# Kernel tuning notes

Hardware: AMD Instinct MI355X
Metric: run time of the kernel (lower is better)

The kernel has to match this reference:

```python
import jax, jax.numpy as jnp
import numpy as np


def setup_inputs() -> dict:
    key = jax.random.key(0)
    k1, k2, k3 = jax.random.split(key, 3)
    B, T, C, H, W = 8, 30, 4, 256, 256
    images = jax.random.normal(k1, (B, T, C, H, W), dtype=jnp.float32)
    # 1 = occluded, 0 = visible (per docstring)
    cloud_mask = jax.random.bernoulli(k2, 0.5, (B, T, 1, H, W)).astype(jnp.float32)
    # strictly increasing acquisition days per batch element
    days = jnp.cumsum(jax.random.randint(k3, (B, T), 1, 10), axis=1).astype(jnp.float32)
    return {"images": images, "cloud_mask": cloud_mask, "days": days}


def _interpolate(images, cloud_mask, days):
    # images: (B,T,C,H,W), cloud_mask: (B,T,1,H,W), days: (B,T)
    B, T, C, H, W = images.shape
    visible = cloud_mask[:, :, 0, :, :] == 0.0                  # (B,T,H,W)
    t_idx = jnp.arange(T, dtype=jnp.int32)[None, :, None, None]

    # last-visible index: running max over time of (t if visible else -1); -1 == never seen yet (NaN in ref)
    lv = jax.lax.cummax(jnp.where(visible, t_idx, -1), axis=1)
    # next-visible index: reverse running min of (t if visible else T); T == never seen again (NaN in ref)
    nv = jax.lax.cummin(jnp.where(visible, t_idx, T), axis=1, reverse=True)

    lv_ok = lv >= 0
    nv_ok = nv < T
    lv_c = jnp.clip(lv, 0, T - 1)
    nv_c = jnp.clip(nv, 0, T - 1)

    def gather_img(idx):  # idx: (B,T,H,W) int -> (B,T,C,H,W)
        full = jnp.broadcast_to(idx[:, :, None, :, :], (B, T, C, H, W))
        return jnp.take_along_axis(images, full, axis=1)

    def gather_day(idx):  # idx: (B,T,H,W) int -> (B,T,H,W)
        return jnp.take_along_axis(days, idx.reshape(B, -1), axis=1).reshape(B, T, H, W)

    img_last = gather_img(lv_c)
    img_next = gather_img(nv_c)
    d_last = gather_day(lv_c)
    d_next = gather_day(nv_c)
    d_t = jnp.broadcast_to(days[:, :, None, None], (B, T, H, W))

    denom = d_next - d_last
    frac = (d_t - d_last) / jnp.where(denom == 0.0, 1.0, denom)  # safe; denom==0 only where visible
    interp = img_last + frac[:, :, None, :, :] * (img_next - img_last)

    vis_c = visible[:, :, None, :, :]
    both = (lv_ok & nv_ok)[:, :, None, :, :]
    only_last = (lv_ok & ~nv_ok)[:, :, None, :, :]
    only_next = (~lv_ok & nv_ok)[:, :, None, :, :]
    nan = jnp.float32(jnp.nan)

    out = jnp.where(vis_c, images,
          jnp.where(both, interp,
          jnp.where(only_last, img_last,
          jnp.where(only_next, img_next, nan))))
    return out


def reference(images, cloud_mask, days):
    return _interpolate(images, cloud_mask, days)
```

## Files before the change

### kernel.cpp

```cpp
#include <hip/hip_runtime.h>

namespace {

constexpr int T   = 30;
constexpr int C   = 4;
constexpr int HW  = 256 * 256;
constexpr int B   = 8;
constexpr int CHW = C * HW;

typedef _Float16 f16x2 __attribute__((ext_vector_type(2)));

__global__ __attribute__((amdgpu_flat_work_group_size(256, 256)))
           __attribute__((amdgpu_waves_per_eu(4, 4)))
void interp_kernel(
    const float* __restrict__ images,
    const float* __restrict__ mask,
    const float* __restrict__ days,
    float* __restrict__ out)
{
    __shared__ float s_day[T];
    const int tid = threadIdx.x;
    const int b   = blockIdx.x >> 8;
    if (tid < T) s_day[tid] = days[b * T + tid];
    __syncthreads();

    const int hw = ((blockIdx.x & 255) << 8) | tid;

    const float* mbase = mask + (size_t)b * T * HW + hw;
    unsigned vis = 0u;
    {
        float mv[T];
#pragma unroll
        for (int t = 0; t < T; ++t) mv[t] = mbase[(size_t)t * HW];
        __builtin_amdgcn_sched_barrier(0);
#pragma unroll
        for (int t = 0; t < T; ++t) vis |= (mv[t] == 0.0f ? 1u : 0u) << t;
    }

    f16x2 fr[T / 2];
    {
        float run = 0.0f;
#pragma unroll
        for (int t = T - 1; t >= 0; --t) {
            run = ((vis >> t) & 1u) ? s_day[t] : run;
            if (t & 1) fr[t >> 1].y = (_Float16)run;
            else       fr[t >> 1].x = (_Float16)run;
        }
        float dl = 0.0f;
#pragma unroll
        for (int t = 0; t < T; ++t) {
            const float d = s_day[t];
            dl = ((vis >> t) & 1u) ? d : dl;
            const float dn = (t & 1) ? (float)fr[t >> 1].y
                                     : (float)fr[t >> 1].x;
            float den = dn - dl;
            den = (den == 0.0f) ? 1.0f : den;
            float f = (d - dl) / den;
            const bool lv_ok = (vis & ((1u << (t + 1)) - 1u)) != 0u;
            const bool nv_ok = (vis >> t) != 0u;
            f = (lv_ok && nv_ok) ? f : (nv_ok ? 1.0f : 0.0f);
            if (t & 1) fr[t >> 1].y = (_Float16)f;
            else       fr[t >> 1].x = (_Float16)f;
        }
    }

    const bool  none = (vis == 0u);
    const float nanv = __int_as_float(0x7fc00000);
    const size_t pixBase = (size_t)b * T * CHW + hw;

#pragma unroll 1
    for (int c = 0; c < C; ++c) {
        const float* ib = images + pixBase + (size_t)c * HW;
        float*       ob = out    + pixBase + (size_t)c * HW;

        float v[T];
#pragma unroll
        for (int t = 0; t < T; ++t) v[t] = ib[(size_t)t * CHW];
        __builtin_amdgcn_sched_barrier(0);

        f16x2 nvp[T / 2];
        {
            float run = 0.0f;
#pragma unroll
            for (int t = T - 1; t >= 0; --t) {
                run = ((vis >> t) & 1u) ? v[t] : run;
                if (t & 1) nvp[t >> 1].y = (_Float16)run;
                else       nvp[t >> 1].x = (_Float16)run;
            }
        }
        {
            float rl = 0.0f;
#pragma unroll
            for (int t = 0; t < T; ++t) {
                const float nv = (t & 1) ? (float)nvp[t >> 1].y
                                         : (float)nvp[t >> 1].x;
                rl = ((vis >> t) & 1u) ? nv : rl;
                const float f  = (t & 1) ? (float)fr[t >> 1].y
                                         : (float)fr[t >> 1].x;
                const float res = fmaf(f, nv - rl, rl);
                __builtin_nontemporal_store(none ? nanv : res,
                                            &ob[(size_t)t * CHW]);
            }
        }
    }
}

}

extern "C" void kernel_launch(void* const* d_in, const int* in_sizes, int n_in,
                              void* d_out, int out_size, void* d_ws, size_t ws_size,
                              hipStream_t stream)
{
    const float* images = (const float*)d_in[0];
    const float* mask   = (const float*)d_in[1];
    const float* days   = (const float*)d_in[2];
    float* out          = (float*)d_out;

    const int nPix = B * HW;
    dim3 grid(nPix / 256), block(256);
    hipLaunchKernelGGL(interp_kernel, grid, block, 0, stream,
                       images, mask, days, out);
}
```

Measured before the change: 108.4 us.

## Double-buffer channel loads to overlap next channel's reads with current scan-store

Replaces the serial per-channel loop with a manually unrolled, double-buffered sequence. The next channel's 30 image values are loaded into a second register array before the current channel's scan and store run, so global load latency overlaps with compute and stores. This roughly doubles the live image registers per thread, which at the fixed 4 waves/EU could cause spills or limit the scheduler.

```diff
diff --git a/kernel.cpp b/kernel.cpp
--- a/kernel.cpp
+++ b/kernel.cpp
@@ -9,6 +9,37 @@
 constexpr int CHW = C * HW;
 
 typedef _Float16 f16x2 __attribute__((ext_vector_type(2)));
+
+__device__ __forceinline__ void scan_store(const float (&v)[T],
+                                           const f16x2 (&fr)[T / 2],
+                                           unsigned vis, bool none,
+                                           float nanv, float* __restrict__ ob)
+{
+    f16x2 nvp[T / 2];
+    {
+        float run = 0.0f;
+#pragma unroll
+        for (int t = T - 1; t >= 0; --t) {
+            run = ((vis >> t) & 1u) ? v[t] : run;
+            if (t & 1) nvp[t >> 1].y = (_Float16)run;
+            else       nvp[t >> 1].x = (_Float16)run;
+        }
+    }
+    {
+        float rl = 0.0f;
+#pragma unroll
+        for (int t = 0; t < T; ++t) {
+            const float nv = (t & 1) ? (float)nvp[t >> 1].y
+                                     : (float)nvp[t >> 1].x;
+            rl = ((vis >> t) & 1u) ? nv : rl;
+            const float f  = (t & 1) ? (float)fr[t >> 1].y
+                                     : (float)fr[t >> 1].x;
+            const float res = fmaf(f, nv - rl, rl);
+            __builtin_nontemporal_store(none ? nanv : res,
+                                        &ob[(size_t)t * CHW]);
+        }
+    }
+}
 
 __global__ __attribute__((amdgpu_flat_work_group_size(256, 256)))
            __attribute__((amdgpu_waves_per_eu(4, 4)))
@@ -25,6 +56,10 @@
     __syncthreads();
 
     const int hw = ((blockIdx.x & 255) << 8) | tid;
+
+    const size_t pixBase = (size_t)b * T * CHW + hw;
+    const float* ib = images + pixBase;
+    float*       ob = out    + pixBase;
 
     const float* mbase = mask + (size_t)b * T * HW + hw;
     unsigned vis = 0u;
@@ -66,43 +101,32 @@
 
     const bool  none = (vis == 0u);
     const float nanv = __int_as_float(0x7fc00000);
-    const size_t pixBase = (size_t)b * T * CHW + hw;
 
-#pragma unroll 1
-    for (int c = 0; c < C; ++c) {
-        const float* ib = images + pixBase + (size_t)c * HW;
-        float*       ob = out    + pixBase + (size_t)c * HW;
+    float va[T], vb[T];
 
-        float v[T];
 #pragma unroll
-        for (int t = 0; t < T; ++t) v[t] = ib[(size_t)t * CHW];
-        __builtin_amdgcn_sched_barrier(0);
+    for (int t = 0; t < T; ++t) va[t] = ib[(size_t)t * CHW];
+    __builtin_amdgcn_sched_barrier(0);
 
-        f16x2 nvp[T / 2];
-        {
-            float run = 0.0f;
 #pragma unroll
-            for (int t = T - 1; t >= 0; --t) {
-                run = ((vis >> t) & 1u) ? v[t] : run;
-                if (t & 1) nvp[t >> 1].y = (_Float16)run;
-                else       nvp[t >> 1].x = (_Float16)run;
-            }
-        }
-        {
-            float rl = 0.0f;
+    for (int t = 0; t < T; ++t) vb[t] = ib[(size_t)t * CHW + HW];
+    __builtin_amdgcn_sched_barrier(0);
+    scan_store(va, fr, vis, none, nanv, ob);
+    __builtin_amdgcn_sched_barrier(0);
+
 #pragma unroll
-            for (int t = 0; t < T; ++t) {
-                const float nv = (t & 1) ? (float)nvp[t >> 1].y
-                                         : (float)nvp[t >> 1].x;
-                rl = ((vis >> t) & 1u) ? nv : rl;
-                const float f  = (t & 1) ? (float)fr[t >> 1].y
-                                         : (float)fr[t >> 1].x;
-                const float res = fmaf(f, nv - rl, rl);
-                __builtin_nontemporal_store(none ? nanv : res,
-                                            &ob[(size_t)t * CHW]);
-            }
-        }
-    }
+    for (int t = 0; t < T; ++t) va[t] = ib[(size_t)t * CHW + 2 * HW];
+    __builtin_amdgcn_sched_barrier(0);
+    scan_store(vb, fr, vis, none, nanv, ob + HW);
+    __builtin_amdgcn_sched_barrier(0);
+
+#pragma unroll
+    for (int t = 0; t < T; ++t) vb[t] = ib[(size_t)t * CHW + 3 * HW];
+    __builtin_amdgcn_sched_barrier(0);
+    scan_store(va, fr, vis, none, nanv, ob + 2 * HW);
+    __builtin_amdgcn_sched_barrier(0);
+
+    scan_store(vb, fr, vis, none, nanv, ob + 3 * HW);
 }
 
 }
```

After: 105.7 us. 2.5% less time.
